# Optimization experiments

Measured on AMD Instinct MI355X. Metric: run time of the kernel, lower is better.

Reference implementation:

```python
import jax, jax.numpy as jnp
import numpy as np

K_VALUES = (2, 4, 8)  # sorted k_values from init


def setup_inputs() -> dict:
    key = jax.random.key(0)
    ks = jax.random.split(key, 6)
    B, T, D, H = 16, 2048, 512, 64
    nk = len(K_VALUES)
    # columns: (E, Pt, eta, phi) -- E,Pt positive, eta in [-3,3], phi in [-pi,pi]
    u = jax.random.uniform(ks[0], (B, T, 4), jnp.float32)
    tokens_cont = u * jnp.array([100.0, 50.0, 6.0, 6.2832], jnp.float32) + jnp.array([1.0, 1.0, -3.0, -3.1416], jnp.float32)
    lengths = jax.random.randint(ks[1], (B,), T // 2, T + 1)
    mask = jnp.arange(T)[None, :] < lengths[:, None]  # [B,T] True=valid
    W1 = jax.random.normal(ks[2], (nk, H), jnp.float32) / np.sqrt(nk).astype(np.float32)
    b1 = jax.random.normal(ks[3], (H,), jnp.float32) * 0.01
    W2 = jax.random.normal(ks[4], (H, D), jnp.float32) / np.sqrt(H).astype(np.float32)
    b2 = jax.random.normal(ks[5], (D,), jnp.float32) * 0.01
    return dict(tokens_cont=tokens_cont, mask=mask, W1=W1, b1=b1, W2=W2, b2=b2)


def reference(tokens_cont, mask, W1, b1, W2, b2):
    B, T, _ = tokens_cont.shape
    E, Pt, eta, phi = (tokens_cont[..., i] for i in range(4))
    px = Pt * jnp.cos(phi)
    py = Pt * jnp.sin(phi)
    pz = Pt * jnp.sinh(jnp.clip(eta, -20.0, 20.0))
    P = jnp.stack([E, px, py, pz], axis=-1)  # [B,T,4] four-momentum
    metric = jnp.array([1.0, -1.0, -1.0, -1.0], P.dtype)
    # Lorentz dot: E_i E_j - px_i px_j - py_i py_j - pz_i pz_j -> [B,T,T]
    dot = jnp.einsum('btc,bsc->bts', P * metric, P)
    dot = jnp.where(mask[:, None, :], dot, -jnp.inf)  # exclude padding friends
    max_k = min(max(K_VALUES), T)
    _, topk_idx = jax.lax.top_k(dot, max_k)  # [B,T,max_k]
    Pf = P[jnp.arange(B)[:, None, None], topk_idx]  # gather friends [B,T,max_k,4]
    cum = jnp.cumsum(Pf, axis=2)  # prefix sums over sorted friends
    masses = []
    maskf = mask.astype(P.dtype)
    for k in K_VALUES:
        ps = cum[:, :, min(k, max_k) - 1, :]  # [B,T,4] summed 4-momentum of top-k group
        m2 = ps[..., 0] ** 2 - jnp.sum(ps[..., 1:] ** 2, axis=-1)
        m2 = jnp.maximum(m2, 0.0) * maskf
        masses.append(jnp.sqrt(m2 + 1e-8))
    mass = jnp.stack(masses, axis=-1)  # [B,T,n_k]
    h = jax.nn.gelu(mass @ W1 + b1, approximate=False)  # torch GELU = exact erf
    return h @ W2 + b2  # [B,T,model_dim]
```

## Files before the change

### kernel.cpp

```cpp
#include <hip/hip_runtime.h>
#include <hip/hip_bf16.h>
#include <math.h>

#define NB 16
#define NT 2048
#define ND 512
#define NH 64

typedef __attribute__((ext_vector_type(8))) short short8;
typedef __attribute__((ext_vector_type(4))) float float4v;

__device__ __forceinline__ bool mask_is_bytes(const int* m) {
    return m[0] == 0x01010101;
}
__device__ __forceinline__ bool mask_at(const int* m, bool bytes, int i) {
    if (bytes) return ((const unsigned char*)m)[i] != 0;
    return m[i] != 0;
}

__device__ __forceinline__ float dot4(float4 a, float4 p) {
    float d = a.x * p.x;
    d = __builtin_fmaf(a.y, p.y, d);
    d = __builtin_fmaf(a.z, p.z, d);
    d = __builtin_fmaf(a.w, p.w, d);
    return d;
}

__device__ __forceinline__ unsigned short f2bf(float x) {
    unsigned int u = __float_as_uint(x);
    u += 0x7fffu + ((u >> 16) & 1u);
    return (unsigned short)(u >> 16);
}

__global__ void __launch_bounds__(256) compute_P_kernel(
        const float* __restrict__ tok,
        const int* __restrict__ mask,
        float4* __restrict__ P,
        unsigned short* __restrict__ W2t,
        const float* __restrict__ W2) {
    const bool mb = mask_is_bytes(mask);
    int i = blockIdx.x * 256 + threadIdx.x;

    float4 t = ((const float4*)tok)[i];
    float E = t.x, Pt = t.y, eta = t.z, phi = t.w;
    float px = Pt * cosf(phi);
    float py = Pt * sinf(phi);
    float pz = Pt * sinhf(fminf(fmaxf(eta, -20.f), 20.f));
    bool m = mask_at(mask, mb, i);
    P[i] = m ? make_float4(E, px, py, pz)
             : make_float4(-1e30f, 0.f, 0.f, 0.f);

    int n = i & 511, k = i >> 9;
    W2t[n * NH + k] = f2bf(W2[k * ND + n]);
}

__global__ void __launch_bounds__(512) topk_mass_kernel(
        const float4* __restrict__ P,
        const int* __restrict__ mask,
        float* __restrict__ massOut) {
    __shared__ float Plds[NT * 4];
    __shared__ float vtop[8][8][64];
    __shared__ float psum[8][12][64];
    __shared__ int wcnt[8];

    const int b    = blockIdx.y;
    const int t0   = blockIdx.x * 64;
    const int tid  = threadIdx.x;
    const int lane = tid & 63;
    const int w    = tid >> 6;
    const bool mb  = mask_is_bytes(mask);

    if (!mask_at(mask, mb, b * NT + t0)) {
        if (tid < 64) {
            float mz = sqrtf(1e-8f);
            int o = (b * NT + t0 + lane) * 3;
            massOut[o + 0] = mz;
            massOut[o + 1] = mz;
            massOut[o + 2] = mz;
        }
        return;
    }

    const float4* Pb = P + b * NT;
    int cnt = 0;
    for (int i = tid; i < NT; i += 512) {
        float4 v = Pb[i];
        *(float4*)&Plds[i * 4] = v;
        cnt += (int)__popcll(__ballot(v.x != -1e30f));
    }
    if (lane == 0) wcnt[w] = cnt;
    __syncthreads();

    int L = 0;
#pragma unroll
    for (int j = 0; j < 8; ++j) L += wcnt[j];
    const int C    = (L + 7) >> 3;
    const int sBeg = w * C;
    const int sEnd = min(sBeg + C, L);

    const int t = t0 + lane;
    const bool maskt = mask_at(mask, mb, b * NT + t);
    float4 pt = *(const float4*)&Plds[(t0 + lane) * 4];
    float4 a  = make_float4(pt.x, -pt.y, -pt.z, -pt.w);

    const float NEGBIG = -3.402823466e38f;
    float v0 = NEGBIG, v1 = NEGBIG, v2 = NEGBIG, v3 = NEGBIG;
    float v4 = NEGBIG, v5 = NEGBIG, v6 = NEGBIG, v7 = NEGBIG;

#pragma unroll 4
    for (int s = sBeg; s < sEnd; ++s) {
        float4 ps = *(const float4*)&Plds[s * 4];
        float d = dot4(a, ps);
        float n0 = fmaxf(v0, d);
        float n1 = __builtin_amdgcn_fmed3f(d, v0, v1);
        float n2 = __builtin_amdgcn_fmed3f(d, v1, v2);
        float n3 = __builtin_amdgcn_fmed3f(d, v2, v3);
        float n4 = __builtin_amdgcn_fmed3f(d, v3, v4);
        float n5 = __builtin_amdgcn_fmed3f(d, v4, v5);
        float n6 = __builtin_amdgcn_fmed3f(d, v5, v6);
        float n7 = __builtin_amdgcn_fmed3f(d, v6, v7);
        v0 = n0; v1 = n1; v2 = n2; v3 = n3;
        v4 = n4; v5 = n5; v6 = n6; v7 = n7;
    }

    vtop[w][0][lane] = v0; vtop[w][1][lane] = v1;
    vtop[w][2][lane] = v2; vtop[w][3][lane] = v3;
    vtop[w][4][lane] = v4; vtop[w][5][lane] = v5;
    vtop[w][6][lane] = v6; vtop[w][7][lane] = v7;
    __syncthreads();

    float m0 = NEGBIG, m1 = NEGBIG, m2_ = NEGBIG, m3 = NEGBIG;
    float m4 = NEGBIG, m5 = NEGBIG, m6 = NEGBIG, m7 = NEGBIG;
#pragma unroll
    for (int w2 = 0; w2 < 8; ++w2) {
#pragma unroll
        for (int j = 0; j < 8; ++j) {
            float d = vtop[w2][j][lane];
            float n0 = fmaxf(m0, d);
            float n1 = __builtin_amdgcn_fmed3f(d, m0, m1);
            float n2 = __builtin_amdgcn_fmed3f(d, m1, m2_);
            float n3 = __builtin_amdgcn_fmed3f(d, m2_, m3);
            float n4 = __builtin_amdgcn_fmed3f(d, m3, m4);
            float n5 = __builtin_amdgcn_fmed3f(d, m4, m5);
            float n6 = __builtin_amdgcn_fmed3f(d, m5, m6);
            float n7 = __builtin_amdgcn_fmed3f(d, m6, m7);
            m0 = n0; m1 = n1; m2_ = n2; m3 = n3;
            m4 = n4; m5 = n5; m6 = n6; m7 = n7;
        }
    }
    const float th2 = m1, th4 = m3, th8 = m7;

    float s2x = 0.f, s2y = 0.f, s2z = 0.f, s2w = 0.f;
    float s4x = 0.f, s4y = 0.f, s4z = 0.f, s4w = 0.f;
    float s8x = 0.f, s8y = 0.f, s8z = 0.f, s8w = 0.f;
#pragma unroll 4
    for (int s = sBeg; s < sEnd; ++s) {
        float4 ps = *(const float4*)&Plds[s * 4];
        float d = dot4(a, ps);
        if (d >= th8) {
            s8x += ps.x; s8y += ps.y; s8z += ps.z; s8w += ps.w;
            if (d >= th4) {
                s4x += ps.x; s4y += ps.y; s4z += ps.z; s4w += ps.w;
                if (d >= th2) {
                    s2x += ps.x; s2y += ps.y; s2z += ps.z; s2w += ps.w;
                }
            }
        }
    }
    psum[w][0][lane] = s2x;  psum[w][1][lane] = s2y;
    psum[w][2][lane] = s2z;  psum[w][3][lane] = s2w;
    psum[w][4][lane] = s4x;  psum[w][5][lane] = s4y;
    psum[w][6][lane] = s4z;  psum[w][7][lane] = s4w;
    psum[w][8][lane] = s8x;  psum[w][9][lane] = s8y;
    psum[w][10][lane] = s8z; psum[w][11][lane] = s8w;
    __syncthreads();

    if (tid < 64) {
        float tot[12];
#pragma unroll
        for (int c = 0; c < 12; ++c) {
            float acc = 0.f;
#pragma unroll
            for (int w2 = 0; w2 < 8; ++w2) acc += psum[w2][c][lane];
            tot[c] = acc;
        }
        auto massf = [&](float sx, float sy, float sz, float sw) -> float {
            float q = sx * sx;
            q = __builtin_fmaf(-sy, sy, q);
            q = __builtin_fmaf(-sz, sz, q);
            q = __builtin_fmaf(-sw, sw, q);
            q = fmaxf(q, 0.f);
            if (!maskt) q = 0.f;
            return sqrtf(q + 1e-8f);
        };
        int o = (b * NT + t) * 3;
        massOut[o + 0] = massf(tot[0], tot[1], tot[2], tot[3]);
        massOut[o + 1] = massf(tot[4], tot[5], tot[6], tot[7]);
        massOut[o + 2] = massf(tot[8], tot[9], tot[10], tot[11]);
    }
}

__global__ void __launch_bounds__(256) mlp_kernel(
        const float* __restrict__ mass,
        const float* __restrict__ W1,
        const float* __restrict__ b1,
        const unsigned short* __restrict__ W2t,
        const float* __restrict__ b2,
        float* __restrict__ out) {
    __shared__ unsigned short hs[32][80];

    const int tid  = threadIdx.x;
    const int lane = tid & 63;
    const int wv   = tid >> 6;
    const int tokBase = blockIdx.x * 32;

    {
        const int tt = tid & 31;
        const int hr = tid >> 5;
        const int tokg = tokBase + tt;
        float m0 = mass[tokg * 3 + 0];
        float m1 = mass[tokg * 3 + 1];
        float m2 = mass[tokg * 3 + 2];
        unsigned short hv[8];
#pragma unroll
        for (int j = 0; j < 8; ++j) {
            int hh = hr * 8 + j;
            float pre = b1[hh];
            pre = __builtin_fmaf(m0, W1[hh], pre);
            pre = __builtin_fmaf(m1, W1[NH + hh], pre);
            pre = __builtin_fmaf(m2, W1[2 * NH + hh], pre);
            float g = 0.5f * pre * (1.0f + erff(pre * 0.70710678118654752f));
            hv[j] = f2bf(g);
        }
        *(short8*)&hs[tt][hr * 8] = *(const short8*)hv;
    }
    __syncthreads();

    const int col  = lane & 15;
    const int quad = lane >> 4;
    const int nBase = wv * 128;

    short8 afrag[2][2];
#pragma unroll
    for (int mt = 0; mt < 2; ++mt)
#pragma unroll
        for (int ks = 0; ks < 2; ++ks)
            afrag[mt][ks] = *(const short8*)&hs[mt * 16 + col][ks * 32 + quad * 8];

    float4v acc[2][8];
#pragma unroll
    for (int mt = 0; mt < 2; ++mt)
#pragma unroll
        for (int nt = 0; nt < 8; ++nt)
            acc[mt][nt] = (float4v)(0.f);

#pragma unroll
    for (int nt = 0; nt < 8; ++nt) {
        const unsigned short* wp = W2t + (nBase + nt * 16 + col) * NH + quad * 8;
        short8 bf0 = *(const short8*)(wp);
        short8 bf1 = *(const short8*)(wp + 32);
        acc[0][nt] = __builtin_amdgcn_mfma_f32_16x16x32_bf16(afrag[0][0], bf0, acc[0][nt], 0, 0, 0);
        acc[1][nt] = __builtin_amdgcn_mfma_f32_16x16x32_bf16(afrag[1][0], bf0, acc[1][nt], 0, 0, 0);
        acc[0][nt] = __builtin_amdgcn_mfma_f32_16x16x32_bf16(afrag[0][1], bf1, acc[0][nt], 0, 0, 0);
        acc[1][nt] = __builtin_amdgcn_mfma_f32_16x16x32_bf16(afrag[1][1], bf1, acc[1][nt], 0, 0, 0);
    }

#pragma unroll
    for (int nt = 0; nt < 8; ++nt) {
        float bias = b2[nBase + nt * 16 + col];
#pragma unroll
        for (int mt = 0; mt < 2; ++mt) {
            int mRow = tokBase + mt * 16 + quad * 4;
            size_t base = (size_t)mRow * ND + nBase + nt * 16 + col;
#pragma unroll
            for (int r = 0; r < 4; ++r) {
                out[base + (size_t)r * ND] = acc[mt][nt][r] + bias;
            }
        }
    }
}

extern "C" void kernel_launch(void* const* d_in, const int* in_sizes, int n_in,
                              void* d_out, int out_size, void* d_ws, size_t ws_size,
                              hipStream_t stream) {
    const float* tok  = (const float*)d_in[0];
    const int*   mask = (const int*)d_in[1];
    const float* W1   = (const float*)d_in[2];
    const float* b1   = (const float*)d_in[3];
    const float* W2   = (const float*)d_in[4];
    const float* b2   = (const float*)d_in[5];
    float*       out  = (float*)d_out;

    float4*         P       = (float4*)d_ws;
    float*          massBuf = (float*)((char*)d_ws + (size_t)NB * NT * 16);
    unsigned short* W2t     = (unsigned short*)((char*)d_ws + (size_t)NB * NT * 16
                                                + (size_t)NB * NT * 3 * 4);

    compute_P_kernel<<<dim3(NB * NT / 256), dim3(256), 0, stream>>>(tok, mask, P, W2t, W2);

    dim3 gB(NT / 64, NB);
    topk_mass_kernel<<<gB, dim3(512), 0, stream>>>(P, mask, massBuf);

    mlp_kernel<<<dim3(NB * NT / 32), dim3(256), 0, stream>>>(massBuf, W1, b1, W2t, b2, out);
}
```

Before: 141.5 us.

## Fuse P computation, top-k mass and MLP into a single kernel

Merges the three-kernel pipeline into one block-per-64-token kernel. Each block computes the four-momenta for its whole batch row into LDS from raw tokens, runs the top-k mass search, then applies the GELU MLP and MFMA projection directly from shared memory. W2 conversion to bf16 moves to a small separate kernel. This removes the global round trips for P and the mass buffer and two launches. In exchange every block redundantly recomputes the trig/sinh for all 2048 tokens of its row, and the larger LDS footprint may lower occupancy.

```diff
diff --git a/kernel.cpp b/kernel.cpp
--- a/kernel.cpp
+++ b/kernel.cpp
@@ -32,35 +32,28 @@
     return (unsigned short)(u >> 16);
 }
 
-__global__ void __launch_bounds__(256) compute_P_kernel(
+__global__ void __launch_bounds__(256) w2t_kernel(
+        const float* __restrict__ W2, unsigned short* __restrict__ W2t) {
+    int i = blockIdx.x * 256 + threadIdx.x;
+    int n = i & (ND - 1), k = i >> 9;
+    W2t[n * NH + k] = f2bf(W2[k * ND + n]);
+}
+
+#define VT(w2, j, l)  scratch[((w2) * 8 + (j)) * 64 + (l)]
+#define PS(w2, c, l)  scratch[((w2) * 12 + (c)) * 64 + (l)]
+
+__global__ void __launch_bounds__(512) fused_topk_mass_mlp_kernel(
         const float* __restrict__ tok,
         const int* __restrict__ mask,
-        float4* __restrict__ P,
-        unsigned short* __restrict__ W2t,
-        const float* __restrict__ W2) {
-    const bool mb = mask_is_bytes(mask);
-    int i = blockIdx.x * 256 + threadIdx.x;
-
-    float4 t = ((const float4*)tok)[i];
-    float E = t.x, Pt = t.y, eta = t.z, phi = t.w;
-    float px = Pt * cosf(phi);
-    float py = Pt * sinf(phi);
-    float pz = Pt * sinhf(fminf(fmaxf(eta, -20.f), 20.f));
-    bool m = mask_at(mask, mb, i);
-    P[i] = m ? make_float4(E, px, py, pz)
-             : make_float4(-1e30f, 0.f, 0.f, 0.f);
-
-    int n = i & 511, k = i >> 9;
-    W2t[n * NH + k] = f2bf(W2[k * ND + n]);
-}
-
-__global__ void __launch_bounds__(512) topk_mass_kernel(
-        const float4* __restrict__ P,
-        const int* __restrict__ mask,
-        float* __restrict__ massOut) {
+        const float* __restrict__ W1,
+        const float* __restrict__ b1,
+        const unsigned short* __restrict__ W2t,
+        const float* __restrict__ b2,
+        float* __restrict__ out) {
     __shared__ float Plds[NT * 4];
-    __shared__ float vtop[8][8][64];
-    __shared__ float psum[8][12][64];
+    __shared__ float scratch[8 * 12 * 64];
+    __shared__ unsigned short hs[64][88];
+    __shared__ float mass_s[3][64];
     __shared__ int wcnt[8];
 
     const int b    = blockIdx.y;
@@ -70,165 +63,156 @@
     const int w    = tid >> 6;
     const bool mb  = mask_is_bytes(mask);
 
-    if (!mask_at(mask, mb, b * NT + t0)) {
+    const bool blockValid = mask_at(mask, mb, b * NT + t0);
+
+    if (blockValid) {
+        int cnt = 0;
+#pragma unroll
+        for (int it = 0; it < 4; ++it) {
+            int i = tid + it * 512;
+            float4 tv = ((const float4*)tok)[b * NT + i];
+            bool m = mask_at(mask, mb, b * NT + i);
+            float E = tv.x, Pt = tv.y, eta = tv.z, phi = tv.w;
+            float px = Pt * cosf(phi);
+            float py = Pt * sinf(phi);
+            float pz = Pt * sinhf(fminf(fmaxf(eta, -20.f), 20.f));
+            float4 pv = m ? make_float4(E, px, py, pz)
+                          : make_float4(-1e30f, 0.f, 0.f, 0.f);
+            *(float4*)&Plds[i * 4] = pv;
+            cnt += (int)__popcll(__ballot(m));
+        }
+        if (lane == 0) wcnt[w] = cnt;
+        __syncthreads();
+
+        int L = 0;
+#pragma unroll
+        for (int j = 0; j < 8; ++j) L += wcnt[j];
+        const int C    = (L + 7) >> 3;
+        const int sBeg = w * C;
+        const int sEnd = min(sBeg + C, L);
+
+        float4 pt = *(const float4*)&Plds[(t0 + lane) * 4];
+        float4 a  = make_float4(pt.x, -pt.y, -pt.z, -pt.w);
+
+        const float NEGBIG = -3.402823466e38f;
+        float v0 = NEGBIG, v1 = NEGBIG, v2 = NEGBIG, v3 = NEGBIG;
+        float v4 = NEGBIG, v5 = NEGBIG, v6 = NEGBIG, v7 = NEGBIG;
+
+#pragma unroll 4
+        for (int s = sBeg; s < sEnd; ++s) {
+            float4 ps = *(const float4*)&Plds[s * 4];
+            float d = dot4(a, ps);
+            float n0 = fmaxf(v0, d);
+            float n1 = __builtin_amdgcn_fmed3f(d, v0, v1);
+            float n2 = __builtin_amdgcn_fmed3f(d, v1, v2);
+            float n3 = __builtin_amdgcn_fmed3f(d, v2, v3);
+            float n4 = __builtin_amdgcn_fmed3f(d, v3, v4);
+            float n5 = __builtin_amdgcn_fmed3f(d, v4, v5);
+            float n6 = __builtin_amdgcn_fmed3f(d, v5, v6);
+            float n7 = __builtin_amdgcn_fmed3f(d, v6, v7);
+            v0 = n0; v1 = n1; v2 = n2; v3 = n3;
+            v4 = n4; v5 = n5; v6 = n6; v7 = n7;
+        }
+        VT(w, 0, lane) = v0; VT(w, 1, lane) = v1;
+        VT(w, 2, lane) = v2; VT(w, 3, lane) = v3;
+        VT(w, 4, lane) = v4; VT(w, 5, lane) = v5;
+        VT(w, 6, lane) = v6; VT(w, 7, lane) = v7;
+        __syncthreads();
+
+        float m0 = NEGBIG, m1 = NEGBIG, m2_ = NEGBIG, m3 = NEGBIG;
+        float m4 = NEGBIG, m5 = NEGBIG, m6 = NEGBIG, m7 = NEGBIG;
+#pragma unroll
+        for (int w2 = 0; w2 < 8; ++w2) {
+#pragma unroll
+            for (int j = 0; j < 8; ++j) {
+                float d = VT(w2, j, lane);
+                float n0 = fmaxf(m0, d);
+                float n1 = __builtin_amdgcn_fmed3f(d, m0, m1);
+                float n2 = __builtin_amdgcn_fmed3f(d, m1, m2_);
+                float n3 = __builtin_amdgcn_fmed3f(d, m2_, m3);
+                float n4 = __builtin_amdgcn_fmed3f(d, m3, m4);
+                float n5 = __builtin_amdgcn_fmed3f(d, m4, m5);
+                float n6 = __builtin_amdgcn_fmed3f(d, m5, m6);
+                float n7 = __builtin_amdgcn_fmed3f(d, m6, m7);
+                m0 = n0; m1 = n1; m2_ = n2; m3 = n3;
+                m4 = n4; m5 = n5; m6 = n6; m7 = n7;
+            }
+        }
+        const float th2 = m1, th4 = m3, th8 = m7;
+        __syncthreads();
+
+        float s2x = 0.f, s2y = 0.f, s2z = 0.f, s2w = 0.f;
+        float s4x = 0.f, s4y = 0.f, s4z = 0.f, s4w = 0.f;
+        float s8x = 0.f, s8y = 0.f, s8z = 0.f, s8w = 0.f;
+#pragma unroll 4
+        for (int s = sBeg; s < sEnd; ++s) {
+            float4 ps = *(const float4*)&Plds[s * 4];
+            float d = dot4(a, ps);
+            if (d >= th8) {
+                s8x += ps.x; s8y += ps.y; s8z += ps.z; s8w += ps.w;
+                if (d >= th4) {
+                    s4x += ps.x; s4y += ps.y; s4z += ps.z; s4w += ps.w;
+                    if (d >= th2) {
+                        s2x += ps.x; s2y += ps.y; s2z += ps.z; s2w += ps.w;
+                    }
+                }
+            }
+        }
+        PS(w, 0, lane) = s2x;  PS(w, 1, lane) = s2y;
+        PS(w, 2, lane) = s2z;  PS(w, 3, lane) = s2w;
+        PS(w, 4, lane) = s4x;  PS(w, 5, lane) = s4y;
+        PS(w, 6, lane) = s4z;  PS(w, 7, lane) = s4w;
+        PS(w, 8, lane) = s8x;  PS(w, 9, lane) = s8y;
+        PS(w, 10, lane) = s8z; PS(w, 11, lane) = s8w;
+        __syncthreads();
+
+        if (w == 0) {
+            float tot[12];
+#pragma unroll
+            for (int c = 0; c < 12; ++c) {
+                float acc = 0.f;
+#pragma unroll
+                for (int w2 = 0; w2 < 8; ++w2) acc += PS(w2, c, lane);
+                tot[c] = acc;
+            }
+            const bool maskt = (t0 + lane) < L;
+            const float MZ = sqrtf(1e-8f);
+            auto massf = [&](float sx, float sy, float sz, float sw) -> float {
+                float q = sx * sx;
+                q = __builtin_fmaf(-sy, sy, q);
+                q = __builtin_fmaf(-sz, sz, q);
+                q = __builtin_fmaf(-sw, sw, q);
+                q = fmaxf(q, 0.f);
+                return sqrtf(q + 1e-8f);
+            };
+            mass_s[0][lane] = maskt ? massf(tot[0], tot[1], tot[2], tot[3]) : MZ;
+            mass_s[1][lane] = maskt ? massf(tot[4], tot[5], tot[6], tot[7]) : MZ;
+            mass_s[2][lane] = maskt ? massf(tot[8], tot[9], tot[10], tot[11]) : MZ;
+        }
+    } else {
         if (tid < 64) {
-            float mz = sqrtf(1e-8f);
-            int o = (b * NT + t0 + lane) * 3;
-            massOut[o + 0] = mz;
-            massOut[o + 1] = mz;
-            massOut[o + 2] = mz;
-        }
-        return;
-    }
-
-    const float4* Pb = P + b * NT;
-    int cnt = 0;
-    for (int i = tid; i < NT; i += 512) {
-        float4 v = Pb[i];
-        *(float4*)&Plds[i * 4] = v;
-        cnt += (int)__popcll(__ballot(v.x != -1e30f));
-    }
-    if (lane == 0) wcnt[w] = cnt;
+            const float MZ = sqrtf(1e-8f);
+            mass_s[0][tid] = MZ;
+            mass_s[1][tid] = MZ;
+            mass_s[2][tid] = MZ;
+        }
+    }
     __syncthreads();
 
-    int L = 0;
-#pragma unroll
-    for (int j = 0; j < 8; ++j) L += wcnt[j];
-    const int C    = (L + 7) >> 3;
-    const int sBeg = w * C;
-    const int sEnd = min(sBeg + C, L);
-
-    const int t = t0 + lane;
-    const bool maskt = mask_at(mask, mb, b * NT + t);
-    float4 pt = *(const float4*)&Plds[(t0 + lane) * 4];
-    float4 a  = make_float4(pt.x, -pt.y, -pt.z, -pt.w);
-
-    const float NEGBIG = -3.402823466e38f;
-    float v0 = NEGBIG, v1 = NEGBIG, v2 = NEGBIG, v3 = NEGBIG;
-    float v4 = NEGBIG, v5 = NEGBIG, v6 = NEGBIG, v7 = NEGBIG;
-
-#pragma unroll 4
-    for (int s = sBeg; s < sEnd; ++s) {
-        float4 ps = *(const float4*)&Plds[s * 4];
-        float d = dot4(a, ps);
-        float n0 = fmaxf(v0, d);
-        float n1 = __builtin_amdgcn_fmed3f(d, v0, v1);
-        float n2 = __builtin_amdgcn_fmed3f(d, v1, v2);
-        float n3 = __builtin_amdgcn_fmed3f(d, v2, v3);
-        float n4 = __builtin_amdgcn_fmed3f(d, v3, v4);
-        float n5 = __builtin_amdgcn_fmed3f(d, v4, v5);
-        float n6 = __builtin_amdgcn_fmed3f(d, v5, v6);
-        float n7 = __builtin_amdgcn_fmed3f(d, v6, v7);
-        v0 = n0; v1 = n1; v2 = n2; v3 = n3;
-        v4 = n4; v5 = n5; v6 = n6; v7 = n7;
-    }
-
-    vtop[w][0][lane] = v0; vtop[w][1][lane] = v1;
-    vtop[w][2][lane] = v2; vtop[w][3][lane] = v3;
-    vtop[w][4][lane] = v4; vtop[w][5][lane] = v5;
-    vtop[w][6][lane] = v6; vtop[w][7][lane] = v7;
-    __syncthreads();
-
-    float m0 = NEGBIG, m1 = NEGBIG, m2_ = NEGBIG, m3 = NEGBIG;
-    float m4 = NEGBIG, m5 = NEGBIG, m6 = NEGBIG, m7 = NEGBIG;
-#pragma unroll
-    for (int w2 = 0; w2 < 8; ++w2) {
-#pragma unroll
-        for (int j = 0; j < 8; ++j) {
-            float d = vtop[w2][j][lane];
-            float n0 = fmaxf(m0, d);
-            float n1 = __builtin_amdgcn_fmed3f(d, m0, m1);
-            float n2 = __builtin_amdgcn_fmed3f(d, m1, m2_);
-            float n3 = __builtin_amdgcn_fmed3f(d, m2_, m3);
-            float n4 = __builtin_amdgcn_fmed3f(d, m3, m4);
-            float n5 = __builtin_amdgcn_fmed3f(d, m4, m5);
-            float n6 = __builtin_amdgcn_fmed3f(d, m5, m6);
-            float n7 = __builtin_amdgcn_fmed3f(d, m6, m7);
-            m0 = n0; m1 = n1; m2_ = n2; m3 = n3;
-            m4 = n4; m5 = n5; m6 = n6; m7 = n7;
-        }
-    }
-    const float th2 = m1, th4 = m3, th8 = m7;
-
-    float s2x = 0.f, s2y = 0.f, s2z = 0.f, s2w = 0.f;
-    float s4x = 0.f, s4y = 0.f, s4z = 0.f, s4w = 0.f;
-    float s8x = 0.f, s8y = 0.f, s8z = 0.f, s8w = 0.f;
-#pragma unroll 4
-    for (int s = sBeg; s < sEnd; ++s) {
-        float4 ps = *(const float4*)&Plds[s * 4];
-        float d = dot4(a, ps);
-        if (d >= th8) {
-            s8x += ps.x; s8y += ps.y; s8z += ps.z; s8w += ps.w;
-            if (d >= th4) {
-                s4x += ps.x; s4y += ps.y; s4z += ps.z; s4w += ps.w;
-                if (d >= th2) {
-                    s2x += ps.x; s2y += ps.y; s2z += ps.z; s2w += ps.w;
-                }
-            }
-        }
-    }
-    psum[w][0][lane] = s2x;  psum[w][1][lane] = s2y;
-    psum[w][2][lane] = s2z;  psum[w][3][lane] = s2w;
-    psum[w][4][lane] = s4x;  psum[w][5][lane] = s4y;
-    psum[w][6][lane] = s4z;  psum[w][7][lane] = s4w;
-    psum[w][8][lane] = s8x;  psum[w][9][lane] = s8y;
-    psum[w][10][lane] = s8z; psum[w][11][lane] = s8w;
-    __syncthreads();
-
-    if (tid < 64) {
-        float tot[12];
-#pragma unroll
-        for (int c = 0; c < 12; ++c) {
-            float acc = 0.f;
-#pragma unroll
-            for (int w2 = 0; w2 < 8; ++w2) acc += psum[w2][c][lane];
-            tot[c] = acc;
-        }
-        auto massf = [&](float sx, float sy, float sz, float sw) -> float {
-            float q = sx * sx;
-            q = __builtin_fmaf(-sy, sy, q);
-            q = __builtin_fmaf(-sz, sz, q);
-            q = __builtin_fmaf(-sw, sw, q);
-            q = fmaxf(q, 0.f);
-            if (!maskt) q = 0.f;
-            return sqrtf(q + 1e-8f);
-        };
-        int o = (b * NT + t) * 3;
-        massOut[o + 0] = massf(tot[0], tot[1], tot[2], tot[3]);
-        massOut[o + 1] = massf(tot[4], tot[5], tot[6], tot[7]);
-        massOut[o + 2] = massf(tot[8], tot[9], tot[10], tot[11]);
-    }
-}
-
-__global__ void __launch_bounds__(256) mlp_kernel(
-        const float* __restrict__ mass,
-        const float* __restrict__ W1,
-        const float* __restrict__ b1,
-        const unsigned short* __restrict__ W2t,
-        const float* __restrict__ b2,
-        float* __restrict__ out) {
-    __shared__ unsigned short hs[32][80];
-
-    const int tid  = threadIdx.x;
-    const int lane = tid & 63;
-    const int wv   = tid >> 6;
-    const int tokBase = blockIdx.x * 32;
-
     {
-        const int tt = tid & 31;
-        const int hr = tid >> 5;
-        const int tokg = tokBase + tt;
-        float m0 = mass[tokg * 3 + 0];
-        float m1 = mass[tokg * 3 + 1];
-        float m2 = mass[tokg * 3 + 2];
+        const int tt = lane;
+        const int hr = w;
+        float q0 = mass_s[0][tt];
+        float q1 = mass_s[1][tt];
+        float q2 = mass_s[2][tt];
         unsigned short hv[8];
 #pragma unroll
         for (int j = 0; j < 8; ++j) {
             int hh = hr * 8 + j;
             float pre = b1[hh];
-            pre = __builtin_fmaf(m0, W1[hh], pre);
-            pre = __builtin_fmaf(m1, W1[NH + hh], pre);
-            pre = __builtin_fmaf(m2, W1[2 * NH + hh], pre);
+            pre = __builtin_fmaf(q0, W1[hh], pre);
+            pre = __builtin_fmaf(q1, W1[NH + hh], pre);
+            pre = __builtin_fmaf(q2, W1[2 * NH + hh], pre);
             float g = 0.5f * pre * (1.0f + erff(pre * 0.70710678118654752f));
             hv[j] = f2bf(g);
         }
@@ -236,16 +220,17 @@
     }
     __syncthreads();
 
-    const int col  = lane & 15;
-    const int quad = lane >> 4;
-    const int nBase = wv * 128;
+    const int col   = lane & 15;
+    const int quad  = lane >> 4;
+    const int mhalf = w >> 2;
+    const int nBase = (w & 3) * 128;
 
     short8 afrag[2][2];
 #pragma unroll
     for (int mt = 0; mt < 2; ++mt)
 #pragma unroll
         for (int ks = 0; ks < 2; ++ks)
-            afrag[mt][ks] = *(const short8*)&hs[mt * 16 + col][ks * 32 + quad * 8];
+            afrag[mt][ks] = *(const short8*)&hs[mhalf * 32 + mt * 16 + col][ks * 32 + quad * 8];
 
     float4v acc[2][8];
 #pragma unroll
@@ -270,7 +255,7 @@
         float bias = b2[nBase + nt * 16 + col];
 #pragma unroll
         for (int mt = 0; mt < 2; ++mt) {
-            int mRow = tokBase + mt * 16 + quad * 4;
+            int mRow = b * NT + t0 + mhalf * 32 + mt * 16 + quad * 4;
             size_t base = (size_t)mRow * ND + nBase + nt * 16 + col;
 #pragma unroll
             for (int r = 0; r < 4; ++r) {
@@ -291,15 +276,11 @@
     const float* b2   = (const float*)d_in[5];
     float*       out  = (float*)d_out;
 
-    float4*         P       = (float4*)d_ws;
-    float*          massBuf = (float*)((char*)d_ws + (size_t)NB * NT * 16);
-    unsigned short* W2t     = (unsigned short*)((char*)d_ws + (size_t)NB * NT * 16
-                                                + (size_t)NB * NT * 3 * 4);
-
-    compute_P_kernel<<<dim3(NB * NT / 256), dim3(256), 0, stream>>>(tok, mask, P, W2t, W2);
+    unsigned short* W2t = (unsigned short*)d_ws;
+
+    w2t_kernel<<<dim3(ND * NH / 256), dim3(256), 0, stream>>>(W2, W2t);
 
     dim3 gB(NT / 64, NB);
-    topk_mass_kernel<<<gB, dim3(512), 0, stream>>>(P, mask, massBuf);
-
-    mlp_kernel<<<dim3(NB * NT / 32), dim3(256), 0, stream>>>(massBuf, W1, b1, W2t, b2, out);
-}
+    fused_topk_mass_mlp_kernel<<<gB, dim3(512), 0, stream>>>(
+        tok, mask, W1, b1, W2t, b2, out);
+}
```

New measurement: 133.6 us. -5.6%, faster.
